# Kernel optimization log

Hardware: AMD Instinct MI355X
Metric: run time of the kernel (lower is better)

The kernel has to match this reference:

```python
import jax, jax.numpy as jnp
import numpy as np

B, N, DIMS, F_DIMS = 4, 16384, 3, 64


def setup_inputs() -> dict:
    key = jax.random.key(0)
    k1, k2, k3 = jax.random.split(key, 3)
    pc = jax.random.normal(k1, (B, N, DIMS), dtype=jnp.float32)
    feats = jax.random.normal(k2, (B, N, F_DIMS), dtype=jnp.float32)
    # single random permutation shared across the batch (tf.random.shuffle(tf.range(N)))
    perm = jax.random.permutation(k3, N).astype(jnp.int32)
    return {"pc": pc, "feats": feats, "perm": perm}


def reference(pc, feats, perm):
    """Faithful JAX port of RandomSample.call.

    pc:    (B, N, dims)   spatial coords
    feats: (B, N, f_dims) features
    perm:  (N,)           random permutation of range(N)
    """
    n = pc.shape[1]
    m = n // 2  # body hardcodes N // 2 regardless of self.scale
    valid_idx = perm[:m]
    invalid_idx = perm[m:]

    valid_pc = jnp.take(pc, valid_idx, axis=1)        # (B, M, dims)
    valid_feats = jnp.take(feats, valid_idx, axis=1)  # (B, M, f_dims)
    invalid_pc = jnp.take(pc, invalid_idx, axis=1)    # (B, M, dims)

    # brute-force KNN: squared euclidean distance of invalid queries vs valid points
    q2 = jnp.sum(invalid_pc * invalid_pc, axis=-1, keepdims=True)   # (B, M, 1)
    p2 = jnp.sum(valid_pc * valid_pc, axis=-1)[:, None, :]          # (B, 1, M)
    cross = jnp.einsum('bqd,bpd->bqp', invalid_pc, valid_pc)        # (B, M, M)
    d2 = q2 - 2.0 * cross + p2                                      # (B, M, M)

    # K=2 nearest; keep the 2nd neighbour index, as in n_idx = knn(...)[:, :, 1]
    _, knn_idx = jax.lax.top_k(-d2, 2)                              # (B, M, 2)
    n_idx = knn_idx[:, :, 1].astype(jnp.int32)                      # (B, M)

    rnds = perm[None, :]  # (1, N), matches tf.expand_dims(shuffle, 0)
    return valid_pc, valid_feats, n_idx, rnds
```

## Files before the change

### kernel.cpp

```cpp
#include <hip/hip_runtime.h>

#define BB 4
#define NN 16384
#define MM 8192
#define FD 64
#define TPB 256
#define QPT 4
#define QPB (TPB * QPT)

#define OUT0 0
#define OUT1 98304
#define OUT2 2195456
#define OUT3 2228224

#define CAND_OFF   0
#define CAND_BYTES ((size_t)BB * MM * 16)
#define CPAIR_OFF  (CAND_OFF + CAND_BYTES)
#define CPAIR_BYTES ((size_t)BB * MM * 8)
#define PART_OFF   (CPAIR_OFF + CPAIR_BYTES)

__device__ __forceinline__ float sumsq3_rn(float x, float y, float z) {
  return __fadd_rn(__fadd_rn(__fmul_rn(x, x), __fmul_rn(y, y)), __fmul_rn(z, z));
}
__device__ __forceinline__ float dist2_rn(float qx, float qy, float qz, float q2,
                                          float4 t) {
  float cross2 = __fmaf_rn(qz, t.z, __fmaf_rn(qy, t.y, __fmul_rn(qx, t.x)));
  return __fadd_rn(__fsub_rn(q2, cross2), t.w);
}
__device__ __forceinline__ double mkkey(float d2, int k) {
  return __hiloint2double(__float_as_int(d2), k);
}
#define KEY_INIT __hiloint2double(0x7F800000, 0x7FFFFFFF)

__global__ __launch_bounds__(256) void gather_kernel(
    const float* __restrict__ pc, const float* __restrict__ feats,
    const int* __restrict__ perm, float* __restrict__ out,
    float4* __restrict__ cand) {
  int idx = blockIdx.x * 256 + threadIdx.x;
  const int F4_TOT = BB * MM * FD / 4;
  const int PTS    = BB * MM;
  if (idx < F4_TOT) {
    int f4 = idx & 15;
    int r  = (idx >> 4) & (MM - 1);
    int b  = idx >> 17;
    int vi = perm[r];
    const float4* src = (const float4*)(feats + ((b * NN + vi) << 6));
    float4* dst = (float4*)(out + OUT1) + idx;
    *dst = src[f4];
  } else if (idx < F4_TOT + PTS) {
    int k = idx - F4_TOT;
    int r = k & (MM - 1);
    int b = k >> 13;
    int vi = perm[r];
    const float* src = pc + (b * NN + vi) * 3;
    float px = src[0], py = src[1], pz = src[2];
    float* dst = out + OUT0 + k * 3;
    dst[0] = px; dst[1] = py; dst[2] = pz;
    cand[k] = make_float4(px + px, py + py, pz + pz, sumsq3_rn(px, py, pz));
  } else if (idx < F4_TOT + PTS + NN) {
    int k = idx - F4_TOT - PTS;
    out[OUT3 + k] = (float)perm[k];
  }
}

__global__ __launch_bounds__(256) void knn_val_kernel(
    const float* __restrict__ pc, const int* __restrict__ perm,
    const float4* __restrict__ cand, float2* __restrict__ part, int nchunk) {
  #pragma clang fp contract(off)
  int c  = blockIdx.x % nchunk;
  int qb = blockIdx.x / nchunk;
  int q0 = qb * QPB + threadIdx.x;
  int b  = qb >> 3;

  float qx[QPT], qy[QPT], qz[QPT], q2[QPT], m1[QPT], m2[QPT];
  #pragma unroll
  for (int s = 0; s < QPT; ++s) {
    int q = q0 + s * TPB;
    int j = q & (MM - 1);
    int qi = perm[MM + j];
    const float* qp = pc + (b * NN + qi) * 3;
    qx[s] = qp[0]; qy[s] = qp[1]; qz[s] = qp[2];
    q2[s] = sumsq3_rn(qx[s], qy[s], qz[s]);
    m1[s] = 3.4e38f; m2[s] = 3.4e38f;
  }

  __shared__ float4 tile[256];

  int span = MM / nchunk;
  int begin = c * span, end = begin + span;

  for (int t0 = begin; t0 < end; t0 += 256) {
    int tlen = min(256, end - t0);
    __syncthreads();
    for (int i = threadIdx.x; i < tlen; i += TPB)
      tile[i] = cand[b * MM + t0 + i];
    __syncthreads();
    #pragma unroll 8
    for (int k = 0; k < tlen; ++k) {
      float4 t = tile[k];
      #pragma unroll
      for (int s = 0; s < QPT; ++s) {
        float d2 = dist2_rn(qx[s], qy[s], qz[s], q2[s], t);
        m2[s] = __builtin_amdgcn_fmed3f(d2, m1[s], m2[s]);
        m1[s] = fminf(d2, m1[s]);
      }
    }
  }

  #pragma unroll
  for (int s = 0; s < QPT; ++s) {
    int q = q0 + s * TPB;
    part[q * nchunk + c] = make_float2(m1[s], m2[s]);
  }
}

__global__ __launch_bounds__(256) void merge_kernel(
    const float2* __restrict__ part, int2* __restrict__ cpair, int nchunk) {
  int q = blockIdx.x * 256 + threadIdx.x;
  double k1 = KEY_INIT, k2 = KEY_INIT;
  for (int c = 0; c < nchunk; ++c) {
    float2 p = part[q * nchunk + c];
    double a = mkkey(p.x, c);
    double d = mkkey(p.y, c);
    k2 = fmin(fmax(a, k1), k2);
    k1 = fmin(a, k1);
    k2 = fmin(fmax(d, k1), k2);
    k1 = fmin(d, k1);
  }
  cpair[q] = make_int2(__double2loint(k1), __double2loint(k2));
}

__global__ __launch_bounds__(256) void recover_kernel(
    const float* __restrict__ pc, const int* __restrict__ perm,
    const float4* __restrict__ cand, const int2* __restrict__ cpair,
    float* __restrict__ out, int nchunk) {
  #pragma clang fp contract(off)
  int wid = threadIdx.x >> 6, lane = threadIdx.x & 63;
  int q = blockIdx.x * 4 + wid;
  int b = q >> 13, j = q & (MM - 1);
  int qi = perm[MM + j];
  const float* qp = pc + (b * NN + qi) * 3;
  float qx = qp[0], qy = qp[1], qz = qp[2];
  float q2 = sumsq3_rn(qx, qy, qz);
  int2 cp = cpair[q];
  int clen = MM / nchunk;
  const float4* cb = cand + (b << 13);

  double m1 = KEY_INIT, m2 = KEY_INIT;
  #pragma unroll
  for (int pass = 0; pass < 2; ++pass) {
    int c = pass == 0 ? cp.x : cp.y;
    if (pass == 1 && cp.y == cp.x) break;
    int base = c * clen;
    for (int i = lane; i < clen; i += 64) {
      float4 t = cb[base + i];
      float d2 = dist2_rn(qx, qy, qz, q2, t);
      double key = mkkey(d2, base + i);
      m2 = fmin(fmax(key, m1), m2);
      m1 = fmin(key, m1);
    }
  }
  #pragma unroll
  for (int mask = 1; mask < 64; mask <<= 1) {
    double o1 = __shfl_xor(m1, mask);
    double o2 = __shfl_xor(m2, mask);
    double n1 = fmin(m1, o1);
    double n2 = fmin(fmax(m1, o1), fmin(m2, o2));
    m1 = n1; m2 = n2;
  }
  if (lane == 0) out[OUT2 + q] = (float)__double2loint(m2);
}

extern "C" void kernel_launch(void* const* d_in, const int* in_sizes, int n_in,
                              void* d_out, int out_size, void* d_ws, size_t ws_size,
                              hipStream_t stream) {
  const float* pc    = (const float*)d_in[0];
  const float* feats = (const float*)d_in[1];
  const int*   perm  = (const int*)d_in[2];
  float* out = (float*)d_out;

  char* ws = (char*)d_ws;
  float4* cand  = (float4*)(ws + CAND_OFF);
  int2*   cpair = (int2*)(ws + CPAIR_OFF);
  float2* part  = (float2*)(ws + PART_OFF);
  size_t  avail = ws_size > PART_OFF ? ws_size - PART_OFF : 0;

  gather_kernel<<<2240, 256, 0, stream>>>(pc, feats, perm, out, cand);

  int nchunk = 8;
  if      (avail >= (size_t)BB * MM * 64 * sizeof(float2)) nchunk = 64;
  else if (avail >= (size_t)BB * MM * 32 * sizeof(float2)) nchunk = 32;
  else if (avail >= (size_t)BB * MM * 16 * sizeof(float2)) nchunk = 16;

  knn_val_kernel<<<(BB * MM / QPB) * nchunk, TPB, 0, stream>>>(pc, perm, cand,
                                                               part, nchunk);
  merge_kernel<<<BB * MM / 256, 256, 0, stream>>>(part, cpair, nchunk);
  recover_kernel<<<BB * MM / 4, 256, 0, stream>>>(pc, perm, cand, cpair, out, nchunk);
}
```

Measured before the change: 78.79 us.

## Vectorize KNN distance with packed float2 math and fuse chunk merge into recover

```diff
diff --git a/kernel.cpp b/kernel.cpp
--- a/kernel.cpp
+++ b/kernel.cpp
@@ -1,4 +1,7 @@
 #include <hip/hip_runtime.h>
+
+typedef float v2f __attribute__((ext_vector_type(2)));
+typedef float v4f __attribute__((ext_vector_type(4)));
 
 #define BB 4
 #define NN 16384
@@ -15,9 +18,7 @@
 
 #define CAND_OFF   0
 #define CAND_BYTES ((size_t)BB * MM * 16)
-#define CPAIR_OFF  (CAND_OFF + CAND_BYTES)
-#define CPAIR_BYTES ((size_t)BB * MM * 8)
-#define PART_OFF   (CPAIR_OFF + CPAIR_BYTES)
+#define PART_OFF   CAND_BYTES
 
 __device__ __forceinline__ float sumsq3_rn(float x, float y, float z) {
   return __fadd_rn(__fadd_rn(__fmul_rn(x, x), __fmul_rn(y, y)), __fmul_rn(z, z));
@@ -72,19 +73,22 @@
   int q0 = qb * QPB + threadIdx.x;
   int b  = qb >> 3;
 
-  float qx[QPT], qy[QPT], qz[QPT], q2[QPT], m1[QPT], m2[QPT];
+  float m1[QPT], m2[QPT];
+  v2f qxp[QPT], qyp[QPT], qzp[QPT], q2p[QPT];
   #pragma unroll
   for (int s = 0; s < QPT; ++s) {
     int q = q0 + s * TPB;
     int j = q & (MM - 1);
     int qi = perm[MM + j];
     const float* qp = pc + (b * NN + qi) * 3;
-    qx[s] = qp[0]; qy[s] = qp[1]; qz[s] = qp[2];
-    q2[s] = sumsq3_rn(qx[s], qy[s], qz[s]);
+    float qx = qp[0], qy = qp[1], qz = qp[2];
+    float q2 = sumsq3_rn(qx, qy, qz);
+    qxp[s] = (v2f){qx, qx}; qyp[s] = (v2f){qy, qy};
+    qzp[s] = (v2f){qz, qz}; q2p[s] = (v2f){q2, q2};
     m1[s] = 3.4e38f; m2[s] = 3.4e38f;
   }
 
-  __shared__ float4 tile[256];
+  __shared__ __align__(16) float lx[256], ly[256], lz[256], lw[256];
 
   int span = MM / nchunk;
   int begin = c * span, end = begin + span;
@@ -92,17 +96,42 @@
   for (int t0 = begin; t0 < end; t0 += 256) {
     int tlen = min(256, end - t0);
     __syncthreads();
-    for (int i = threadIdx.x; i < tlen; i += TPB)
-      tile[i] = cand[b * MM + t0 + i];
+    if (threadIdx.x < tlen) {
+      float4 t = cand[b * MM + t0 + threadIdx.x];
+      lx[threadIdx.x] = t.x; ly[threadIdx.x] = t.y;
+      lz[threadIdx.x] = t.z; lw[threadIdx.x] = t.w;
+    }
     __syncthreads();
-    #pragma unroll 8
-    for (int k = 0; k < tlen; ++k) {
-      float4 t = tile[k];
+    #pragma unroll 2
+    for (int k = 0; k < tlen; k += 4) {
+      v4f x4 = *(const v4f*)&lx[k];
+      v4f y4 = *(const v4f*)&ly[k];
+      v4f z4 = *(const v4f*)&lz[k];
+      v4f w4 = *(const v4f*)&lw[k];
+      v2f xa = __builtin_shufflevector(x4, x4, 0, 1);
+      v2f xb = __builtin_shufflevector(x4, x4, 2, 3);
+      v2f ya = __builtin_shufflevector(y4, y4, 0, 1);
+      v2f yb = __builtin_shufflevector(y4, y4, 2, 3);
+      v2f za = __builtin_shufflevector(z4, z4, 0, 1);
+      v2f zb = __builtin_shufflevector(z4, z4, 2, 3);
+      v2f wa = __builtin_shufflevector(w4, w4, 0, 1);
+      v2f wb = __builtin_shufflevector(w4, w4, 2, 3);
       #pragma unroll
       for (int s = 0; s < QPT; ++s) {
-        float d2 = dist2_rn(qx[s], qy[s], qz[s], q2[s], t);
-        m2[s] = __builtin_amdgcn_fmed3f(d2, m1[s], m2[s]);
-        m1[s] = fminf(d2, m1[s]);
+        v2f crA = __builtin_elementwise_fma(qzp[s], za,
+                  __builtin_elementwise_fma(qyp[s], ya, qxp[s] * xa));
+        v2f dA  = (q2p[s] - crA) + wa;
+        m2[s] = __builtin_amdgcn_fmed3f(dA.x, m1[s], m2[s]);
+        m1[s] = fminf(dA.x, m1[s]);
+        m2[s] = __builtin_amdgcn_fmed3f(dA.y, m1[s], m2[s]);
+        m1[s] = fminf(dA.y, m1[s]);
+        v2f crB = __builtin_elementwise_fma(qzp[s], zb,
+                  __builtin_elementwise_fma(qyp[s], yb, qxp[s] * xb));
+        v2f dB  = (q2p[s] - crB) + wb;
+        m2[s] = __builtin_amdgcn_fmed3f(dB.x, m1[s], m2[s]);
+        m1[s] = fminf(dB.x, m1[s]);
+        m2[s] = __builtin_amdgcn_fmed3f(dB.y, m1[s], m2[s]);
+        m1[s] = fminf(dB.y, m1[s]);
       }
     }
   }
@@ -114,25 +143,9 @@
   }
 }
 
-__global__ __launch_bounds__(256) void merge_kernel(
-    const float2* __restrict__ part, int2* __restrict__ cpair, int nchunk) {
-  int q = blockIdx.x * 256 + threadIdx.x;
-  double k1 = KEY_INIT, k2 = KEY_INIT;
-  for (int c = 0; c < nchunk; ++c) {
-    float2 p = part[q * nchunk + c];
-    double a = mkkey(p.x, c);
-    double d = mkkey(p.y, c);
-    k2 = fmin(fmax(a, k1), k2);
-    k1 = fmin(a, k1);
-    k2 = fmin(fmax(d, k1), k2);
-    k1 = fmin(d, k1);
-  }
-  cpair[q] = make_int2(__double2loint(k1), __double2loint(k2));
-}
-
 __global__ __launch_bounds__(256) void recover_kernel(
     const float* __restrict__ pc, const int* __restrict__ perm,
-    const float4* __restrict__ cand, const int2* __restrict__ cpair,
+    const float4* __restrict__ cand, const float2* __restrict__ part,
     float* __restrict__ out, int nchunk) {
   #pragma clang fp contract(off)
   int wid = threadIdx.x >> 6, lane = threadIdx.x & 63;
@@ -142,15 +155,31 @@
   const float* qp = pc + (b * NN + qi) * 3;
   float qx = qp[0], qy = qp[1], qz = qp[2];
   float q2 = sumsq3_rn(qx, qy, qz);
-  int2 cp = cpair[q];
+
+  double k1 = KEY_INIT, k2 = KEY_INIT;
+  if (lane < nchunk) {
+    float2 p = part[q * nchunk + lane];
+    k1 = mkkey(p.x, lane);
+    k2 = mkkey(p.y, lane);
+  }
+  #pragma unroll
+  for (int mask = 1; mask < 64; mask <<= 1) {
+    double o1 = __shfl_xor(k1, mask);
+    double o2 = __shfl_xor(k2, mask);
+    double n1 = fmin(k1, o1);
+    double n2 = fmin(fmax(k1, o1), fmin(k2, o2));
+    k1 = n1; k2 = n2;
+  }
+  int c1 = __double2loint(k1);
+  int c2 = __double2loint(k2);
+
   int clen = MM / nchunk;
   const float4* cb = cand + (b << 13);
-
   double m1 = KEY_INIT, m2 = KEY_INIT;
   #pragma unroll
   for (int pass = 0; pass < 2; ++pass) {
-    int c = pass == 0 ? cp.x : cp.y;
-    if (pass == 1 && cp.y == cp.x) break;
+    int c = pass == 0 ? c1 : c2;
+    if (pass == 1 && c2 == c1) break;
     int base = c * clen;
     for (int i = lane; i < clen; i += 64) {
       float4 t = cb[base + i];
@@ -180,9 +209,8 @@
   float* out = (float*)d_out;
 
   char* ws = (char*)d_ws;
-  float4* cand  = (float4*)(ws + CAND_OFF);
-  int2*   cpair = (int2*)(ws + CPAIR_OFF);
-  float2* part  = (float2*)(ws + PART_OFF);
+  float4* cand = (float4*)(ws + CAND_OFF);
+  float2* part = (float2*)(ws + PART_OFF);
   size_t  avail = ws_size > PART_OFF ? ws_size - PART_OFF : 0;
 
   gather_kernel<<<2240, 256, 0, stream>>>(pc, feats, perm, out, cand);
@@ -194,6 +222,5 @@
 
   knn_val_kernel<<<(BB * MM / QPB) * nchunk, TPB, 0, stream>>>(pc, perm, cand,
                                                                part, nchunk);
-  merge_kernel<<<BB * MM / 256, 256, 0, stream>>>(part, cpair, nchunk);
-  recover_kernel<<<BB * MM / 4, 256, 0, stream>>>(pc, perm, cand, cpair, out, nchunk);
-}
+  recover_kernel<<<BB * MM / 4, 256, 0, stream>>>(pc, perm, cand, part, out, nchunk);
+}
```

Result: faster. 76.95 us (-2.3%).
